# Kernel tuning notes

Hardware: AMD Instinct MI355X
Metric: run time of the kernel (lower is better)

## Reference

```python
import jax, jax.numpy as jnp
import numpy as np

N = 100000      # total nodes
G = 500         # graphs
NPG = 200       # nodes per graph
E = 1_600_000   # edges
XS = 128        # input feature dim
FIX = 10        # fixed_size one-hot id dim
H = 64          # hidden (neuron)
NPERM = 3
YS = 1


def setup_inputs() -> dict:
    key = jax.random.key(0)
    ks = jax.random.split(key, 10)
    x = jax.random.normal(ks[0], (N, XS), jnp.float32)

    rng = np.random.default_rng(0)
    src = rng.integers(0, N, E)
    off = rng.integers(1, NPG, E)
    dst = (src // NPG) * NPG + (src % NPG + off) % NPG  # edges stay within graph
    edge_index = jnp.asarray(np.stack([src, dst]).astype(np.int32))
    batch_ids = jnp.asarray((np.arange(N) // NPG).astype(np.int32))

    # permuted tiled-eye node ids: node at local pos p gets one_hot(perm[p] % 10)
    base = np.arange(NPG) % FIX  # tiled eye row indices for one graph
    ids = rng.permuted(np.tile(base, (NPERM, G, 1)), axis=-1).reshape(NPERM, N)
    perm_ids = jax.nn.one_hot(jnp.asarray(ids), FIX, dtype=jnp.float32)

    def lin(k, fin, fout):
        return jax.random.normal(k, (fin, fout), jnp.float32) * (1.0 / np.sqrt(fin))

    return {
        "x": x, "edge_index": edge_index, "batch_ids": batch_ids, "perm_ids": perm_ids,
        "w1": lin(ks[1], XS + FIX, H), "b1": jnp.zeros((H,), jnp.float32),
        "w2": lin(ks[2], H, H), "b2": jnp.zeros((H,), jnp.float32),
        "w3": lin(ks[3], H, H), "b3": jnp.zeros((H,), jnp.float32),
        "a1w": lin(ks[4], H, 16), "a1b": jnp.zeros((16,), jnp.float32),
        "a2w": lin(ks[5], 16, YS), "a2b": jnp.zeros((YS,), jnp.float32),
    }


def reference(x, edge_index, batch_ids, perm_ids,
              w1, b1, w2, b2, w3, b3, a1w, a1b, a2w, a2b):
    src, dst = edge_index[0], edge_index[1]
    loop = jnp.arange(N, dtype=src.dtype)
    src_a = jnp.concatenate([src, loop])  # GCNConv adds self-loops
    dst_a = jnp.concatenate([dst, loop])
    deg = jax.ops.segment_sum(jnp.ones_like(dst_a, x.dtype), dst_a, N)
    dinv = jnp.where(deg > 0, deg ** -0.5, 0.0)
    norm = (dinv[src_a] * dinv[dst_a])[:, None]  # [E+N, 1]

    def conv(h, W, b):
        h = h @ W  # transform first (cheaper: H <= in_dim)
        return jax.ops.segment_sum(h[src_a] * norm, dst_a, N) + b

    counts = jnp.maximum(jax.ops.segment_sum(jnp.ones((N,), x.dtype), batch_ids, G), 1.0)

    out = jnp.zeros((G, H), x.dtype)
    for p in range(NPERM):
        h = jnp.concatenate([x, perm_ids[p]], axis=1)  # [N, XS+FIX]
        h = jax.nn.relu(conv(h, w1, b1))
        h = jax.nn.relu(conv(h, w2, b2))
        h = jax.nn.relu(conv(h, w3, b3))
        hg = jax.ops.segment_sum(h, batch_ids, G) / counts[:, None]  # mean pool
        out = out + hg / NPERM

    out = jax.nn.relu(out @ a1w + a1b)
    return out @ a2w + a2b  # [G, YS]
```

## Files before the change

### kernel.cpp

```cpp
#include <hip/hip_runtime.h>

#define NN   100000
#define EE   1600000
#define GG   500
#define NPGc 200
#define HH   64
#define NPERMc 3
#define C1   16384
#define HST  74
#define BSTRIDE 4096

typedef __fp16   h16x2 __attribute__((ext_vector_type(2)));
typedef _Float16 f16x4 __attribute__((ext_vector_type(4)));
typedef _Float16 f16x8 __attribute__((ext_vector_type(8)));
typedef float    f32x4 __attribute__((ext_vector_type(4)));

__device__ __forceinline__ void cvt_hilo(f32x4 a, f32x4 b, f16x8& hi, f16x8& lo) {
    float f[8] = {a[0], a[1], a[2], a[3], b[0], b[1], b[2], b[3]};
#pragma unroll
    for (int j = 0; j < 8; j += 2) {
        h16x2 h = __builtin_amdgcn_cvt_pkrtz(f[j], f[j + 1]);
        h16x2 l = __builtin_amdgcn_cvt_pkrtz(f[j] - (float)h[0], f[j + 1] - (float)h[1]);
        hi[j] = (_Float16)h[0]; hi[j + 1] = (_Float16)h[1];
        lo[j] = (_Float16)l[0]; lo[j + 1] = (_Float16)l[1];
    }
}

__device__ __forceinline__ void cvt_hilo4(const float (&v)[4], f16x4& hv, f16x4& lv) {
#pragma unroll
    for (int i = 0; i < 4; i += 2) {
        h16x2 h = __builtin_amdgcn_cvt_pkrtz(v[i], v[i + 1]);
        h16x2 l = __builtin_amdgcn_cvt_pkrtz(v[i] - (float)h[0], v[i + 1] - (float)h[1]);
        hv[i] = (_Float16)h[0]; hv[i + 1] = (_Float16)h[1];
        lv[i] = (_Float16)l[0]; lv[i + 1] = (_Float16)l[1];
    }
}

#define EB 98
__global__ __launch_bounds__(512) void k_prep(const int* __restrict__ ei, int* __restrict__ gcnt,
                                              unsigned short* __restrict__ gtok,
                                              const float* __restrict__ w1, const float* __restrict__ w2,
                                              const float* __restrict__ w3, _Float16* __restrict__ wf) {
    int t = threadIdx.x;
    if (blockIdx.x >= EB) {
        int tid = (blockIdx.x - EB) * 512 + t;
        int c = tid >> 6, lane = tid & 63;
        int q = lane >> 4, m = lane & 15;
        const float* src; int kstep, ct, term;
        if (c < 32) { kstep = c & 3; ct = (c >> 2) & 3; term = c >> 4; src = w1; }
        else {
            int c2 = c - 32;
            kstep = c2 & 1; ct = (c2 >> 1) & 3; term = (c2 >> 3) & 1;
            src = (c2 >> 4) ? w3 : w2;
        }
        f16x8 v;
#pragma unroll
        for (int j = 0; j < 8; ++j) {
            int k = kstep * 32 + q * 8 + j;
            int n = ct * 16 + m;
            float wv = src[k * 64 + n];
            _Float16 hi = (_Float16)wv;
            float lo = wv - (float)hi;
            v[j] = term ? (_Float16)lo : hi;
        }
        *((f16x8*)(wf + c * 512) + lane) = v;
        return;
    }
    __shared__ unsigned short stag[C1];
    __shared__ int h[512], esc[512], cur[512], gb[512];
    int base = blockIdx.x * C1;
    int nE = min(C1, EE - base);
    h[t] = 0; cur[t] = 0;
    __syncthreads();
    for (int i = t; i < nE; i += 512) atomicAdd(&h[ei[base + i] / NPGc], 1);
    __syncthreads();
    esc[t] = h[t];
    __syncthreads();
    for (int off = 1; off < 512; off <<= 1) {
        int u = (t >= off) ? esc[t - off] : 0;
        __syncthreads();
        esc[t] += u;
        __syncthreads();
    }
    esc[t] -= h[t];
    if (t < GG && h[t] > 0) gb[t] = atomicAdd(&gcnt[t], h[t]);
    __syncthreads();
    for (int i = t; i < nE; i += 512) {
        int s = ei[base + i], d = ei[EE + base + i];
        int g = s / NPGc;
        int ls = s - g * NPGc, ld = d - g * NPGc;
        int pos = esc[g] + atomicAdd(&cur[g], 1);
        stag[pos] = (unsigned short)(ls | (ld << 8));
    }
    __syncthreads();
    int w = t >> 6, lane = t & 63;
    for (int g = w; g < GG; g += 8) {
        int c = h[g]; if (!c) continue;
        int lb = esc[g], off = gb[g];
        int lim = min(c, BSTRIDE - off);
        for (int j = lane; j < lim; j += 64) gtok[(size_t)g * BSTRIDE + off + j] = stag[lb + j];
    }
}

__global__ __launch_bounds__(256) void k_xw(const float* __restrict__ x,
                                            const _Float16* __restrict__ wf,
                                            float* __restrict__ xW) {
    int lane = threadIdx.x & 63, w = threadIdx.x >> 6;
    int rbase = blockIdx.x * 64 + w * 16;
    int m = lane & 15, q = lane >> 4;
    int row = rbase + m;
    int rowc = min(row, NN - 1);
    f16x8 Ah[4], Al[4];
#pragma unroll
    for (int ks = 0; ks < 4; ++ks) {
        const float* ar = x + (size_t)rowc * 128 + ks * 32 + q * 8;
        f32x4 f0 = *(const f32x4*)ar;
        f32x4 f1 = *(const f32x4*)(ar + 4);
        cvt_hilo(f0, f1, Ah[ks], Al[ks]);
    }
#pragma unroll
    for (int ct = 0; ct < 4; ++ct) {
        f32x4 acc = {0.f, 0.f, 0.f, 0.f};
#pragma unroll
        for (int ks = 0; ks < 4; ++ks) {
            f16x8 Bh = *((const f16x8*)(wf + ((0 * 4 + ct) * 4 + ks) * 512) + lane);
            f16x8 Bl = *((const f16x8*)(wf + ((1 * 4 + ct) * 4 + ks) * 512) + lane);
            acc = __builtin_amdgcn_mfma_f32_16x16x32_f16(Ah[ks], Bh, acc, 0, 0, 0);
            acc = __builtin_amdgcn_mfma_f32_16x16x32_f16(Al[ks], Bh, acc, 0, 0, 0);
            acc = __builtin_amdgcn_mfma_f32_16x16x32_f16(Ah[ks], Bl, acc, 0, 0, 0);
        }
#pragma unroll
        for (int i = 0; i < 4; ++i) {
            int r = rbase + q * 4 + i;
            if (r < NN) xW[(size_t)r * 64 + ct * 16 + m] = acc[i];
        }
    }
}

__device__ __forceinline__ f16x8 cvt_a8(uint2 v) {
    f16x8 r;
#pragma unroll
    for (int k = 0; k < 4; ++k) r[k] = (_Float16)(float)((v.x >> (8 * k)) & 255u);
#pragma unroll
    for (int k = 0; k < 4; ++k) r[4 + k] = (_Float16)(float)((v.y >> (8 * k)) & 255u);
    return r;
}

template <bool POOL>
__device__ __forceinline__ void conv_mfma(const _Float16* __restrict__ Tfh,
                                          const _Float16* __restrict__ Tfl,
                                          float* __restrict__ H,
                                          const f16x8 (&Af)[2][7], int w, int m, int q, int nmt,
                                          const float (&dvv)[2][4], const float (&bias)[4],
                                          float (&poolv)[4]) {
    f32x4 acc[2][4];
#pragma unroll
    for (int mi = 0; mi < 2; ++mi)
#pragma unroll
        for (int ct = 0; ct < 4; ++ct) acc[mi][ct] = (f32x4){0.f, 0.f, 0.f, 0.f};
    int lane = m + 16 * q;
    for (int ks = 0; ks < 7; ++ks) {
#pragma unroll
        for (int ct = 0; ct < 4; ++ct) {
            f16x8 Bh = *((const f16x8*)(Tfh + (ks * 4 + ct) * 512) + lane);
            f16x8 Bl = *((const f16x8*)(Tfl + (ks * 4 + ct) * 512) + lane);
            acc[0][ct] = __builtin_amdgcn_mfma_f32_16x16x32_f16(Af[0][ks], Bh, acc[0][ct], 0, 0, 0);
            acc[0][ct] = __builtin_amdgcn_mfma_f32_16x16x32_f16(Af[0][ks], Bl, acc[0][ct], 0, 0, 0);
            if (nmt > 1) {
                acc[1][ct] = __builtin_amdgcn_mfma_f32_16x16x32_f16(Af[1][ks], Bh, acc[1][ct], 0, 0, 0);
                acc[1][ct] = __builtin_amdgcn_mfma_f32_16x16x32_f16(Af[1][ks], Bl, acc[1][ct], 0, 0, 0);
            }
        }
    }
#pragma unroll
    for (int mi = 0; mi < 2; ++mi) {
        if (mi >= nmt) break;
        int rbase = (w + 8 * mi) * 16 + q * 4;
#pragma unroll
        for (int ct = 0; ct < 4; ++ct) {
            if (!POOL) {
#pragma unroll
                for (int i = 0; i < 4; ++i)
                    H[(rbase + i) * HST + ct * 16 + m] =
                        fmaxf(fmaf(dvv[mi][i], acc[mi][ct][i], bias[ct]), 0.f);
            } else {
                float pl = 0.f;
#pragma unroll
                for (int i = 0; i < 4; ++i) {
                    float o = fmaxf(fmaf(dvv[mi][i], acc[mi][ct][i], bias[ct]), 0.f);
                    if (rbase + i < NPGc) pl += o;
                }
                poolv[ct] += pl;
            }
        }
    }
}

__device__ __forceinline__ void gemm_mfma(const float* __restrict__ H,
                                          _Float16* __restrict__ Tfh, _Float16* __restrict__ Tfl,
                                          const _Float16* __restrict__ wf, int w, int lane,
                                          int m, int q, int nmt, const float (&dvv)[2][4]) {
#pragma unroll
    for (int mi = 0; mi < 2; ++mi) {
        if (mi >= nmt) break;
        int mt = w + 8 * mi;
        f16x8 Ah[2], Al[2];
#pragma unroll
        for (int ks = 0; ks < 2; ++ks) {
            const float* ap = H + (mt * 16 + m) * HST + ks * 32 + 8 * q;
            float2 u0 = *(const float2*)ap;
            float2 u1 = *(const float2*)(ap + 2);
            float2 u2 = *(const float2*)(ap + 4);
            float2 u3 = *(const float2*)(ap + 6);
            f32x4 a = {u0.x, u0.y, u1.x, u1.y};
            f32x4 b = {u2.x, u2.y, u3.x, u3.y};
            cvt_hilo(a, b, Ah[ks], Al[ks]);
        }
        int quad = ((mt & 1) << 1) + (q >> 1);
        int j0 = (q & 1) << 2;
        int lanep = m + (quad << 4);
#pragma unroll
        for (int ct = 0; ct < 4; ++ct) {
            f32x4 acc = {0.f, 0.f, 0.f, 0.f};
#pragma unroll
            for (int ks = 0; ks < 2; ++ks) {
                f16x8 Bh = *((const f16x8*)(wf + ((0 * 4 + ct) * 2 + ks) * 512) + lane);
                f16x8 Bl = *((const f16x8*)(wf + ((1 * 4 + ct) * 2 + ks) * 512) + lane);
                acc = __builtin_amdgcn_mfma_f32_16x16x32_f16(Ah[ks], Bh, acc, 0, 0, 0);
                acc = __builtin_amdgcn_mfma_f32_16x16x32_f16(Al[ks], Bh, acc, 0, 0, 0);
                acc = __builtin_amdgcn_mfma_f32_16x16x32_f16(Ah[ks], Bl, acc, 0, 0, 0);
            }
            float o[4];
#pragma unroll
            for (int i = 0; i < 4; ++i) o[i] = acc[i] * dvv[mi][i];
            f16x4 hv, lv;
            cvt_hilo4(o, hv, lv);
            int off = ((mt >> 1) * 4 + ct) * 512 + lanep * 8 + j0;
            *(f16x4*)(Tfh + off) = hv;
            *(f16x4*)(Tfl + off) = lv;
        }
    }
}

__global__ __launch_bounds__(512, 2) void k_fused(
    const float* __restrict__ xW, const float* __restrict__ perm,
    const float* __restrict__ w1tail,
    const float* __restrict__ b1, const float* __restrict__ b2, const float* __restrict__ b3,
    const _Float16* __restrict__ wsW23,
    const int* __restrict__ gcnt, const unsigned short* __restrict__ gtok,
    const float* __restrict__ a1w, const float* __restrict__ a1b,
    const float* __restrict__ a2w, const float* __restrict__ a2b,
    float* __restrict__ out) {
    __shared__ __align__(16) float Hm[15392];
    __shared__ __align__(16) _Float16 Tfh[28 * 512];
    __shared__ __align__(16) _Float16 Tfl[28 * 512];
    __shared__ __align__(16) _Float16 wlds[16384];
    __shared__ float w1r[640];
    __shared__ float dv[224];
    __shared__ float pool[8 * 64];
    __shared__ unsigned char idsl[672];

    unsigned char* A8  = (unsigned char*)Hm;
    unsigned int*  A32 = (unsigned int*)Hm;

    int g = blockIdx.x, t = threadIdx.x;
    int lane = t & 63, w = t >> 6;
    int m = lane & 15, q = lane >> 4;
    int nbase = g * NPGc;
    int cnt = min(gcnt[g], BSTRIDE);
    const unsigned short* tok = gtok + (size_t)g * BSTRIDE;

    for (int i = t; i < 2048; i += 512) ((f16x8*)wlds)[i] = ((const f16x8*)wsW23)[i];
    for (int i = t; i < 640; i += 512) w1r[i] = w1tail[i];
    for (int i = t; i < 2912; i += 512) ((uint4*)A8)[i] = make_uint4(0, 0, 0, 0);
    __syncthreads();
    for (int i = t; i < cnt; i += 512) {
        int tk = tok[i];
        int addr = (tk >> 8) * 224 + (tk & 255);
        atomicAdd(&A32[addr >> 2], 1u << ((addr & 3) * 8));
    }
    if (t < NPGc) { int a = t * 225; atomicAdd(&A32[a >> 2], 1u << ((a & 3) * 8)); }
    for (int i = t; i < 672; i += 512) {
        int p = i / 224, nd = i - p * 224;
        int id = 0;
        if (nd < NPGc) {
            const float* pp = perm + ((size_t)p * NN + nbase + nd) * 10;
            float best = pp[0];
#pragma unroll
            for (int k = 1; k < 10; ++k) { float v = pp[k]; if (v > best) { best = v; id = k; } }
        }
        idsl[i] = (unsigned char)id;
    }
    __syncthreads();
    if (t < 224) {
        unsigned s = 0;
        if (t < 208)
            for (int i = 0; i < 56; ++i) {
                unsigned v = A32[t * 56 + i];
                s += (v & 255u) + ((v >> 8) & 255u) + ((v >> 16) & 255u) + (v >> 24);
            }
        dv[t] = s ? rsqrtf((float)s) : 0.f;
    }
    int nmt = (w < 5) ? 2 : 1;
    f16x8 Af[2][7];
#pragma unroll
    for (int mi = 0; mi < 2; ++mi) {
        int mt = w + 8 * mi;
        if (mt < 13) {
#pragma unroll
            for (int ks = 0; ks < 7; ++ks) {
                uint2 v = *(const uint2*)(A8 + (mt * 16 + m) * 224 + ks * 32 + q * 8);
                Af[mi][ks] = cvt_a8(v);
            }
        }
    }
    __syncthreads();

    float dvv[2][4];
#pragma unroll
    for (int mi = 0; mi < 2; ++mi)
#pragma unroll
        for (int i = 0; i < 4; ++i) {
            int r = (w + 8 * mi) * 16 + q * 4 + i;
            dvv[mi][i] = (w + 8 * mi < 13) ? dv[r] : 0.f;
        }
    float bb1[4], bb2[4], bb3[4];
#pragma unroll
    for (int ct = 0; ct < 4; ++ct) {
        bb1[ct] = b1[ct * 16 + m]; bb2[ct] = b2[ct * 16 + m]; bb3[ct] = b3[ct * 16 + m];
    }

    float poolv[4] = {0.f, 0.f, 0.f, 0.f};

    for (int p = 0; p < NPERMc; ++p) {
        {
            const unsigned char* ids = idsl + p * 224;
            for (int nd0 = w * 28; nd0 < w * 28 + 28; nd0 += 4) {
                float vals[4];
#pragma unroll
                for (int i = 0; i < 4; ++i) {
                    int nd = nd0 + i;
                    float v = 0.f;
                    if (nd < NPGc) {
                        int id = ids[nd];
                        v = dv[nd] * (xW[(size_t)(nbase + nd) * 64 + lane] + w1r[id * 64 + lane]);
                    }
                    vals[i] = v;
                }
                f16x4 hv, lv;
                cvt_hilo4(vals, hv, lv);
                int c = (nd0 >> 5) * 4 + (lane >> 4);
                int lanep = (lane & 15) + (((nd0 & 31) >> 3) << 4);
                int off = c * 512 + lanep * 8 + (nd0 & 7);
                *(f16x4*)(Tfh + off) = hv;
                *(f16x4*)(Tfl + off) = lv;
            }
        }
        __syncthreads();
        conv_mfma<false>(Tfh, Tfl, Hm, Af, w, m, q, nmt, dvv, bb1, poolv);
        __syncthreads();
        gemm_mfma(Hm, Tfh, Tfl, wlds, w, lane, m, q, nmt, dvv);
        __syncthreads();
        conv_mfma<false>(Tfh, Tfl, Hm, Af, w, m, q, nmt, dvv, bb2, poolv);
        __syncthreads();
        gemm_mfma(Hm, Tfh, Tfl, wlds + 8192, w, lane, m, q, nmt, dvv);
        __syncthreads();
        conv_mfma<true>(Tfh, Tfl, Hm, Af, w, m, q, nmt, dvv, bb3, poolv);
        __syncthreads();
    }

#pragma unroll
    for (int ct = 0; ct < 4; ++ct) {
        float v = poolv[ct];
        v += __shfl_xor(v, 16);
        v += __shfl_xor(v, 32);
        if (q == 0) pool[w * 64 + ct * 16 + m] = v;
    }
    __syncthreads();
    if (t < 64) {
        float tot = 0.f;
#pragma unroll
        for (int i = 0; i < 8; ++i) tot += pool[i * 64 + t];
        pool[t] = tot * (1.0f / (NPGc * NPERMc));
    }
    __syncthreads();
    if (t < 16) {
        float a = a1b[t];
        for (int k = 0; k < 64; ++k) a = fmaf(pool[k], a1w[k * 16 + t], a);
        pool[64 + t] = fmaxf(a, 0.f);
    }
    __syncthreads();
    if (t == 0) {
        float o = a2b[0];
#pragma unroll
        for (int i = 0; i < 16; ++i) o = fmaf(pool[64 + i], a2w[i], o);
        out[g] = o;
    }
}


static inline size_t alignup(size_t x) { return (x + 255) & ~(size_t)255; }

extern "C" void kernel_launch(void* const* d_in, const int* in_sizes, int n_in,
                              void* d_out, int out_size, void* d_ws, size_t ws_size,
                              hipStream_t stream) {
    const float* x    = (const float*)d_in[0];
    const int*   ei   = (const int*)d_in[1];
    const float* perm = (const float*)d_in[3];
    const float* w1   = (const float*)d_in[4];
    const float* b1   = (const float*)d_in[5];
    const float* w2   = (const float*)d_in[6];
    const float* b2   = (const float*)d_in[7];
    const float* w3   = (const float*)d_in[8];
    const float* b3   = (const float*)d_in[9];
    const float* a1w  = (const float*)d_in[10];
    const float* a1b  = (const float*)d_in[11];
    const float* a2w  = (const float*)d_in[12];
    const float* a2b  = (const float*)d_in[13];
    float* out = (float*)d_out;

    char* p = (char*)d_ws;
    auto take = [&](size_t bytes) { char* r = p; p += alignup(bytes); return r; };
    float*          xW   = (float*)take((size_t)NN * 64 * 4);
    unsigned short* gtok = (unsigned short*)take((size_t)GG * BSTRIDE * 2);
    _Float16*       wsW  = (_Float16*)take((size_t)64 * 512 * 2);
    int*            gcnt = (int*)take(512 * 4);
    (void)hipMemsetAsync(gcnt, 0, 512 * 4, stream);

    k_prep<<<EB + 8, 512, 0, stream>>>(ei, gcnt, gtok, w1, w2, w3, wsW);
    k_xw<<<(NN + 63) / 64, 256, 0, stream>>>(x, wsW, xW);
    k_fused<<<GG, 512, 0, stream>>>(xW, perm, w1 + 128 * 64, b1, b2, b3,
                                    wsW + 32 * 512, gcnt, gtok,
                                    a1w, a1b, a2w, a2b, out);
}
```

Baseline: 277.4 us.

## Merge edge bucketing and x@W1 into one launch; retile fused conv warps 4x2

Merges the edge-bucketing prep kernel and the x@W1 MFMA kernel into a single launch. Each x@W1 block builds the W1 hi/lo fp16 fragments in LDS itself, and k_fused builds the W2/W3 fragments from the fp32 weights, so the workspace weight buffer and one kernel launch go away. Inside k_fused the warp tiling changes from 8 warps each owning all 4 column tiles to a 4x2 grid, where each warp owns 3-4 row tiles and 2 column tiles. This halves the B-fragment LDS reads per warp but keeps more A fragments in registers, which may pressure occupancy under launch_bounds(512,2). The W1 fragments are also rebuilt redundantly in every xW block.

```diff
diff --git a/kernel.cpp b/kernel.cpp
--- a/kernel.cpp
+++ b/kernel.cpp
@@ -9,6 +9,8 @@
 #define C1   16384
 #define HST  74
 #define BSTRIDE 4096
+#define EB   98
+#define XWB  782
 
 typedef __fp16   h16x2 __attribute__((ext_vector_type(2)));
 typedef _Float16 f16x4 __attribute__((ext_vector_type(4)));
@@ -36,38 +38,69 @@
     }
 }
 
-#define EB 98
-__global__ __launch_bounds__(512) void k_prep(const int* __restrict__ ei, int* __restrict__ gcnt,
-                                              unsigned short* __restrict__ gtok,
-                                              const float* __restrict__ w1, const float* __restrict__ w2,
-                                              const float* __restrict__ w3, _Float16* __restrict__ wf) {
+__device__ __forceinline__ f16x8 wfrag_slot(const float* __restrict__ src, int kstep, int ct,
+                                            int term, int mq, int qq) {
+    f16x8 v;
+#pragma unroll
+    for (int j = 0; j < 8; ++j) {
+        float wv = src[(kstep * 32 + qq * 8 + j) * 64 + ct * 16 + mq];
+        _Float16 hi = (_Float16)wv;
+        v[j] = term ? (_Float16)(wv - (float)hi) : hi;
+    }
+    return v;
+}
+
+__global__ __launch_bounds__(512) void k_pre(const int* __restrict__ ei, int* __restrict__ gcnt,
+                                             unsigned short* __restrict__ gtok,
+                                             const float* __restrict__ w1,
+                                             const float* __restrict__ x, float* __restrict__ xW) {
+    __shared__ __align__(16) char shmem[40960];
     int t = threadIdx.x;
+
     if (blockIdx.x >= EB) {
-        int tid = (blockIdx.x - EB) * 512 + t;
-        int c = tid >> 6, lane = tid & 63;
-        int q = lane >> 4, m = lane & 15;
-        const float* src; int kstep, ct, term;
-        if (c < 32) { kstep = c & 3; ct = (c >> 2) & 3; term = c >> 4; src = w1; }
-        else {
-            int c2 = c - 32;
-            kstep = c2 & 1; ct = (c2 >> 1) & 3; term = (c2 >> 3) & 1;
-            src = (c2 >> 4) ? w3 : w2;
-        }
-        f16x8 v;
-#pragma unroll
-        for (int j = 0; j < 8; ++j) {
-            int k = kstep * 32 + q * 8 + j;
-            int n = ct * 16 + m;
-            float wv = src[k * 64 + n];
-            _Float16 hi = (_Float16)wv;
-            float lo = wv - (float)hi;
-            v[j] = term ? (_Float16)lo : hi;
-        }
-        *((f16x8*)(wf + c * 512) + lane) = v;
+        _Float16* wfl = (_Float16*)shmem;
+        for (int i = t; i < 2048; i += 512) {
+            int c = i >> 6, lane2 = i & 63;
+            ((f16x8*)wfl)[i] = wfrag_slot(w1, c & 3, (c >> 2) & 3, c >> 4, lane2 & 15, lane2 >> 4);
+        }
+        __syncthreads();
+        int lane = t & 63, w = t >> 6;
+        int rbase = (blockIdx.x - EB) * 128 + w * 16;
+        int m = lane & 15, q = lane >> 4;
+        int rowc = min(rbase + m, NN - 1);
+        f16x8 Ah[4], Al[4];
+#pragma unroll
+        for (int ks = 0; ks < 4; ++ks) {
+            const float* ar = x + (size_t)rowc * 128 + ks * 32 + q * 8;
+            f32x4 f0 = *(const f32x4*)ar;
+            f32x4 f1 = *(const f32x4*)(ar + 4);
+            cvt_hilo(f0, f1, Ah[ks], Al[ks]);
+        }
+#pragma unroll
+        for (int ct = 0; ct < 4; ++ct) {
+            f32x4 acc = {0.f, 0.f, 0.f, 0.f};
+#pragma unroll
+            for (int ks = 0; ks < 4; ++ks) {
+                f16x8 Bh = ((const f16x8*)wfl)[((0 * 4 + ct) * 4 + ks) * 64 + lane];
+                f16x8 Bl = ((const f16x8*)wfl)[((1 * 4 + ct) * 4 + ks) * 64 + lane];
+                acc = __builtin_amdgcn_mfma_f32_16x16x32_f16(Ah[ks], Bh, acc, 0, 0, 0);
+                acc = __builtin_amdgcn_mfma_f32_16x16x32_f16(Al[ks], Bh, acc, 0, 0, 0);
+                acc = __builtin_amdgcn_mfma_f32_16x16x32_f16(Ah[ks], Bl, acc, 0, 0, 0);
+            }
+#pragma unroll
+            for (int i = 0; i < 4; ++i) {
+                int r = rbase + q * 4 + i;
+                if (r < NN) xW[(size_t)r * 64 + ct * 16 + m] = acc[i];
+            }
+        }
         return;
     }
-    __shared__ unsigned short stag[C1];
-    __shared__ int h[512], esc[512], cur[512], gb[512];
+
+    unsigned short* stag = (unsigned short*)shmem;
+    int* h   = (int*)(shmem + 32768);
+    int* esc = h + 512;
+    int* cur = esc + 512;
+    int* gb  = cur + 512;
     int base = blockIdx.x * C1;
     int nE = min(C1, EE - base);
     h[t] = 0; cur[t] = 0;
@@ -102,41 +135,6 @@
     }
 }
 
-__global__ __launch_bounds__(256) void k_xw(const float* __restrict__ x,
-                                            const _Float16* __restrict__ wf,
-                                            float* __restrict__ xW) {
-    int lane = threadIdx.x & 63, w = threadIdx.x >> 6;
-    int rbase = blockIdx.x * 64 + w * 16;
-    int m = lane & 15, q = lane >> 4;
-    int row = rbase + m;
-    int rowc = min(row, NN - 1);
-    f16x8 Ah[4], Al[4];
-#pragma unroll
-    for (int ks = 0; ks < 4; ++ks) {
-        const float* ar = x + (size_t)rowc * 128 + ks * 32 + q * 8;
-        f32x4 f0 = *(const f32x4*)ar;
-        f32x4 f1 = *(const f32x4*)(ar + 4);
-        cvt_hilo(f0, f1, Ah[ks], Al[ks]);
-    }
-#pragma unroll
-    for (int ct = 0; ct < 4; ++ct) {
-        f32x4 acc = {0.f, 0.f, 0.f, 0.f};
-#pragma unroll
-        for (int ks = 0; ks < 4; ++ks) {
-            f16x8 Bh = *((const f16x8*)(wf + ((0 * 4 + ct) * 4 + ks) * 512) + lane);
-            f16x8 Bl = *((const f16x8*)(wf + ((1 * 4 + ct) * 4 + ks) * 512) + lane);
-            acc = __builtin_amdgcn_mfma_f32_16x16x32_f16(Ah[ks], Bh, acc, 0, 0, 0);
-            acc = __builtin_amdgcn_mfma_f32_16x16x32_f16(Al[ks], Bh, acc, 0, 0, 0);
-            acc = __builtin_amdgcn_mfma_f32_16x16x32_f16(Ah[ks], Bl, acc, 0, 0, 0);
-        }
-#pragma unroll
-        for (int i = 0; i < 4; ++i) {
-            int r = rbase + q * 4 + i;
-            if (r < NN) xW[(size_t)r * 64 + ct * 16 + m] = acc[i];
-        }
-    }
-}
-
 __device__ __forceinline__ f16x8 cvt_a8(uint2 v) {
     f16x8 r;
 #pragma unroll
@@ -150,44 +148,48 @@
 __device__ __forceinline__ void conv_mfma(const _Float16* __restrict__ Tfh,
                                           const _Float16* __restrict__ Tfl,
                                           float* __restrict__ H,
-                                          const f16x8 (&Af)[2][7], int w, int m, int q, int nmt,
-                                          const float (&dvv)[2][4], const float (&bias)[4],
+                                          const f16x8 (&Af)[4][7], int lane, int m, int q,
+                                          int wn, int mtbase, int nmt,
+                                          const float (&dvv)[4][4], const float (&bias)[4],
                                           float (&poolv)[4]) {
-    f32x4 acc[2][4];
-#pragma unroll
-    for (int mi = 0; mi < 2; ++mi)
-#pragma unroll
-        for (int ct = 0; ct < 4; ++ct) acc[mi][ct] = (f32x4){0.f, 0.f, 0.f, 0.f};
-    int lane = m + 16 * q;
+    f32x4 acc[4][2];
+#pragma unroll
+    for (int mi = 0; mi < 4; ++mi)
+#pragma unroll
+        for (int c = 0; c < 2; ++c) acc[mi][c] = (f32x4){0.f, 0.f, 0.f, 0.f};
+
+#pragma unroll
     for (int ks = 0; ks < 7; ++ks) {
 #pragma unroll
-        for (int ct = 0; ct < 4; ++ct) {
-            f16x8 Bh = *((const f16x8*)(Tfh + (ks * 4 + ct) * 512) + lane);
-            f16x8 Bl = *((const f16x8*)(Tfl + (ks * 4 + ct) * 512) + lane);
-            acc[0][ct] = __builtin_amdgcn_mfma_f32_16x16x32_f16(Af[0][ks], Bh, acc[0][ct], 0, 0, 0);
-            acc[0][ct] = __builtin_amdgcn_mfma_f32_16x16x32_f16(Af[0][ks], Bl, acc[0][ct], 0, 0, 0);
-            if (nmt > 1) {
-                acc[1][ct] = __builtin_amdgcn_mfma_f32_16x16x32_f16(Af[1][ks], Bh, acc[1][ct], 0, 0, 0);
-                acc[1][ct] = __builtin_amdgcn_mfma_f32_16x16x32_f16(Af[1][ks], Bl, acc[1][ct], 0, 0, 0);
-            }
-        }
-    }
-#pragma unroll
-    for (int mi = 0; mi < 2; ++mi) {
+        for (int c = 0; c < 2; ++c) {
+            int ct = wn * 2 + c;
+            f16x8 Bh = ((const f16x8*)Tfh)[(ks * 4 + ct) * 64 + lane];
+            f16x8 Bl = ((const f16x8*)Tfl)[(ks * 4 + ct) * 64 + lane];
+#pragma unroll
+            for (int mi = 0; mi < 4; ++mi) {
+                if (mi >= nmt) break;
+                acc[mi][c] = __builtin_amdgcn_mfma_f32_16x16x32_f16(Af[mi][ks], Bh, acc[mi][c], 0, 0, 0);
+                acc[mi][c] = __builtin_amdgcn_mfma_f32_16x16x32_f16(Af[mi][ks], Bl, acc[mi][c], 0, 0, 0);
+            }
+        }
+    }
+#pragma unroll
+    for (int mi = 0; mi < 4; ++mi) {
         if (mi >= nmt) break;
-        int rbase = (w + 8 * mi) * 16 + q * 4;
-#pragma unroll
-        for (int ct = 0; ct < 4; ++ct) {
+        int rbase = (mtbase + mi) * 16 + q * 4;
+#pragma unroll
+        for (int c = 0; c < 2; ++c) {
+            int ct = wn * 2 + c;
             if (!POOL) {
 #pragma unroll
                 for (int i = 0; i < 4; ++i)
                     H[(rbase + i) * HST + ct * 16 + m] =
-                        fmaxf(fmaf(dvv[mi][i], acc[mi][ct][i], bias[ct]), 0.f);
+                        fmaxf(fmaf(dvv[mi][i], acc[mi][c][i], bias[ct]), 0.f);
             } else {
                 float pl = 0.f;
 #pragma unroll
                 for (int i = 0; i < 4; ++i) {
-                    float o = fmaxf(fmaf(dvv[mi][i], acc[mi][ct][i], bias[ct]), 0.f);
+                    float o = fmaxf(fmaf(dvv[mi][i], acc[mi][c][i], bias[ct]), 0.f);
                     if (rbase + i < NPGc) pl += o;
                 }
                 poolv[ct] += pl;
@@ -198,12 +200,13 @@
 
 __device__ __forceinline__ void gemm_mfma(const float* __restrict__ H,
                                           _Float16* __restrict__ Tfh, _Float16* __restrict__ Tfl,
-                                          const _Float16* __restrict__ wf, int w, int lane,
-                                          int m, int q, int nmt, const float (&dvv)[2][4]) {
-#pragma unroll
-    for (int mi = 0; mi < 2; ++mi) {
+                                          const _Float16* __restrict__ wf, int lane,
+                                          int m, int q, int wn, int mtbase, int nmt,
+                                          const float (&dvv)[4][4]) {
+#pragma unroll
+    for (int mi = 0; mi < 4; ++mi) {
         if (mi >= nmt) break;
-        int mt = w + 8 * mi;
+        int mt = mtbase + mi;
         f16x8 Ah[2], Al[2];
 #pragma unroll
         for (int ks = 0; ks < 2; ++ks) {
@@ -216,16 +219,17 @@
             f32x4 b = {u2.x, u2.y, u3.x, u3.y};
             cvt_hilo(a, b, Ah[ks], Al[ks]);
         }
-        int quad = ((mt & 1) << 1) + (q >> 1);
+        int quad = (2 * mt + (q >> 1)) & 3;
         int j0 = (q & 1) << 2;
         int lanep = m + (quad << 4);
 #pragma unroll
-        for (int ct = 0; ct < 4; ++ct) {
+        for (int c = 0; c < 2; ++c) {
+            int ct = wn * 2 + c;
             f32x4 acc = {0.f, 0.f, 0.f, 0.f};
 #pragma unroll
             for (int ks = 0; ks < 2; ++ks) {
-                f16x8 Bh = *((const f16x8*)(wf + ((0 * 4 + ct) * 2 + ks) * 512) + lane);
-                f16x8 Bl = *((const f16x8*)(wf + ((1 * 4 + ct) * 2 + ks) * 512) + lane);
+                f16x8 Bh = ((const f16x8*)wf)[((0 * 4 + ct) * 2 + ks) * 64 + lane];
+                f16x8 Bl = ((const f16x8*)wf)[((1 * 4 + ct) * 2 + ks) * 64 + lane];
                 acc = __builtin_amdgcn_mfma_f32_16x16x32_f16(Ah[ks], Bh, acc, 0, 0, 0);
                 acc = __builtin_amdgcn_mfma_f32_16x16x32_f16(Al[ks], Bh, acc, 0, 0, 0);
                 acc = __builtin_amdgcn_mfma_f32_16x16x32_f16(Ah[ks], Bl, acc, 0, 0, 0);
@@ -244,9 +248,9 @@
 
 __global__ __launch_bounds__(512, 2) void k_fused(
     const float* __restrict__ xW, const float* __restrict__ perm,
-    const float* __restrict__ w1tail,
+    const float* __restrict__ w1,
     const float* __restrict__ b1, const float* __restrict__ b2, const float* __restrict__ b3,
-    const _Float16* __restrict__ wsW23,
+    const float* __restrict__ w2, const float* __restrict__ w3,
     const int* __restrict__ gcnt, const unsigned short* __restrict__ gtok,
     const float* __restrict__ a1w, const float* __restrict__ a1b,
     const float* __restrict__ a2w, const float* __restrict__ a2b,
@@ -254,7 +258,7 @@
     __shared__ __align__(16) float Hm[15392];
     __shared__ __align__(16) _Float16 Tfh[28 * 512];
     __shared__ __align__(16) _Float16 Tfl[28 * 512];
-    __shared__ __align__(16) _Float16 wlds[16384];
+    __shared__ __align__(16) _Float16 wlds[32 * 512];
     __shared__ float w1r[640];
     __shared__ float dv[224];
     __shared__ float pool[8 * 64];
@@ -266,12 +270,20 @@
     int g = blockIdx.x, t = threadIdx.x;
     int lane = t & 63, w = t >> 6;
     int m = lane & 15, q = lane >> 4;
+    int wm = w >> 1, wn = w & 1;
+    int mtbase = (wm == 0) ? 0 : 3 * wm + 1;
+    int nmt = (wm == 0) ? 4 : 3;
     int nbase = g * NPGc;
     int cnt = min(gcnt[g], BSTRIDE);
     const unsigned short* tok = gtok + (size_t)g * BSTRIDE;
 
-    for (int i = t; i < 2048; i += 512) ((f16x8*)wlds)[i] = ((const f16x8*)wsW23)[i];
-    for (int i = t; i < 640; i += 512) w1r[i] = w1tail[i];
+    for (int i = t; i < 2048; i += 512) {
+        int c = i >> 6, lane2 = i & 63;
+        const float* src = (c >= 16) ? w3 : w2;
+        int c4 = c & 15;
+        ((f16x8*)wlds)[i] = wfrag_slot(src, c4 & 1, (c4 >> 1) & 3, c4 >> 3, lane2 & 15, lane2 >> 4);
+    }
+    for (int i = t; i < 640; i += 512) w1r[i] = w1[128 * 64 + i];
     for (int i = t; i < 2912; i += 512) ((uint4*)A8)[i] = make_uint4(0, 0, 0, 0);
     __syncthreads();
     for (int i = t; i < cnt; i += 512) {
@@ -301,29 +313,24 @@
             }
         dv[t] = s ? rsqrtf((float)s) : 0.f;
     }
-    int nmt = (w < 5) ? 2 : 1;
-    f16x8 Af[2][7];
-#pragma unroll
-    for (int mi = 0; mi < 2; ++mi) {
-        int mt = w + 8 * mi;
-        if (mt < 13) {
-#pragma unroll
-            for (int ks = 0; ks < 7; ++ks) {
-                uint2 v = *(const uint2*)(A8 + (mt * 16 + m) * 224 + ks * 32 + q * 8);
-                Af[mi][ks] = cvt_a8(v);
-            }
-        }
-    }
-    __syncthreads();
-
-    float dvv[2][4];
-#pragma unroll
-    for (int mi = 0; mi < 2; ++mi)
-#pragma unroll
-        for (int i = 0; i < 4; ++i) {
-            int r = (w + 8 * mi) * 16 + q * 4 + i;
-            dvv[mi][i] = (w + 8 * mi < 13) ? dv[r] : 0.f;
-        }
+    f16x8 Af[4][7];
+#pragma unroll
+    for (int mi = 0; mi < 4; ++mi) {
+        if (mi >= nmt) break;
+#pragma unroll
+        for (int ks = 0; ks < 7; ++ks) {
+            uint2 v = *(const uint2*)(A8 + ((mtbase + mi) * 16 + m) * 224 + ks * 32 + q * 8);
+            Af[mi][ks] = cvt_a8(v);
+        }
+    }
+    __syncthreads();
+
+    float dvv[4][4];
+#pragma unroll
+    for (int mi = 0; mi < 4; ++mi)
+#pragma unroll
+        for (int i = 0; i < 4; ++i)
+            dvv[mi][i] = (mi < nmt) ? dv[(mtbase + mi) * 16 + q * 4 + i] : 0.f;
     float bb1[4], bb2[4], bb3[4];
 #pragma unroll
     for (int ct = 0; ct < 4; ++ct) {
@@ -357,15 +364,15 @@
             }
         }
         __syncthreads();
-        conv_mfma<false>(Tfh, Tfl, Hm, Af, w, m, q, nmt, dvv, bb1, poolv);
-        __syncthreads();
-        gemm_mfma(Hm, Tfh, Tfl, wlds, w, lane, m, q, nmt, dvv);
-        __syncthreads();
-        conv_mfma<false>(Tfh, Tfl, Hm, Af, w, m, q, nmt, dvv, bb2, poolv);
-        __syncthreads();
-        gemm_mfma(Hm, Tfh, Tfl, wlds + 8192, w, lane, m, q, nmt, dvv);
-        __syncthreads();
-        conv_mfma<true>(Tfh, Tfl, Hm, Af, w, m, q, nmt, dvv, bb3, poolv);
+        conv_mfma<false>(Tfh, Tfl, Hm, Af, lane, m, q, wn, mtbase, nmt, dvv, bb1, poolv);
+        __syncthreads();
+        gemm_mfma(Hm, Tfh, Tfl, wlds, lane, m, q, wn, mtbase, nmt, dvv);
+        __syncthreads();
+        conv_mfma<false>(Tfh, Tfl, Hm, Af, lane, m, q, wn, mtbase, nmt, dvv, bb2, poolv);
+        __syncthreads();
+        gemm_mfma(Hm, Tfh, Tfl, wlds + 16 * 512, lane, m, q, wn, mtbase, nmt, dvv);
+        __syncthreads();
+        conv_mfma<true>(Tfh, Tfl, Hm, Af, lane, m, q, wn, mtbase, nmt, dvv, bb3, poolv);
         __syncthreads();
     }
 
@@ -423,13 +430,10 @@
     auto take = [&](size_t bytes) { char* r = p; p += alignup(bytes); return r; };
     float*          xW   = (float*)take((size_t)NN * 64 * 4);
     unsigned short* gtok = (unsigned short*)take((size_t)GG * BSTRIDE * 2);
-    _Float16*       wsW  = (_Float16*)take((size_t)64 * 512 * 2);
     int*            gcnt = (int*)take(512 * 4);
     (void)hipMemsetAsync(gcnt, 0, 512 * 4, stream);
 
-    k_prep<<<EB + 8, 512, 0, stream>>>(ei, gcnt, gtok, w1, w2, w3, wsW);
-    k_xw<<<(NN + 63) / 64, 256, 0, stream>>>(x, wsW, xW);
-    k_fused<<<GG, 512, 0, stream>>>(xW, perm, w1 + 128 * 64, b1, b2, b3,
-                                    wsW + 32 * 512, gcnt, gtok,
-                                    a1w, a1b, a2w, a2b, out);
-}
+    k_pre<<<EB + XWB, 512, 0, stream>>>(ei, gcnt, gtok, w1, x, xW);
+    k_fused<<<GG, 512, 0, stream>>>(xW, perm, w1, b1, b2, b3, w2, w3,
+                                    gcnt, gtok, a1w, a1b, a2w, a2b, out);
+}
```

New measurement: 358.6 us. 1.29x slower.
